# Kernel tuning notes

Measured on AMD Instinct MI355X. Metric: run time of the kernel, lower is better.

## Reference

```python
import jax, jax.numpy as jnp
import numpy as np

EMBED_DIM = 1024
NUM_HEADS = 16
D_K = EMBED_DIM // NUM_HEADS


def setup_inputs() -> dict:
    key = jax.random.key(0)
    ks = jax.random.split(key, 9)
    s = 1.0 / np.sqrt(EMBED_DIM)
    x = jax.random.normal(ks[0], (4, 2048, EMBED_DIM), dtype=jnp.float32)
    # nn.Linear weights stored as [out, in]; we keep [in, out] for x @ W
    W_q = jax.random.uniform(ks[1], (EMBED_DIM, EMBED_DIM), jnp.float32, -s, s)
    b_q = jax.random.uniform(ks[2], (EMBED_DIM,), jnp.float32, -s, s)
    W_k = jax.random.uniform(ks[3], (EMBED_DIM, EMBED_DIM), jnp.float32, -s, s)
    b_k = jax.random.uniform(ks[4], (EMBED_DIM,), jnp.float32, -s, s)
    W_v = jax.random.uniform(ks[5], (EMBED_DIM, EMBED_DIM), jnp.float32, -s, s)
    b_v = jax.random.uniform(ks[6], (EMBED_DIM,), jnp.float32, -s, s)
    W_o = jax.random.uniform(ks[7], (EMBED_DIM, EMBED_DIM), jnp.float32, -s, s)
    b_o = jax.random.uniform(ks[8], (EMBED_DIM,), jnp.float32, -s, s)
    return {"x": x, "W_q": W_q, "b_q": b_q, "W_k": W_k, "b_k": b_k,
            "W_v": W_v, "b_v": b_v, "W_o": W_o, "b_o": b_o}


def reference(x, W_q, b_q, W_k, b_k, W_v, b_v, W_o, b_o):
    B, N, _ = x.shape
    # QKV projections, split into heads: [B, H, N, d_k]
    def proj(W, b):
        return (x @ W + b).reshape(B, N, NUM_HEADS, D_K).transpose(0, 2, 1, 3)
    Q, K, V = proj(W_q, b_q), proj(W_k, b_k), proj(W_v, b_v)
    scale = 1.0 / np.sqrt(D_K).astype(np.float32)
    scores = jnp.einsum('bhqd,bhkd->bhqk', Q, K) * scale  # [B,H,N,N]
    weights = jax.nn.softmax(scores, axis=-1)
    # dropout is identity in eval mode
    attn = jnp.einsum('bhqk,bhkd->bhqd', weights, V)  # [B,H,N,d_k]
    attn = attn.transpose(0, 2, 1, 3).reshape(B, N, EMBED_DIM)
    return attn @ W_o + b_o
```

## Files before the change

### kernel.cpp

```cpp
#include <hip/hip_runtime.h>

typedef __bf16 bf16;
typedef __attribute__((ext_vector_type(8))) __bf16 bf16x8;
typedef __attribute__((ext_vector_type(4))) __bf16 bf16x4;
typedef __attribute__((ext_vector_type(4))) float f32x4;

static __device__ __forceinline__ f32x4 mfma16(bf16x8 a, bf16x8 b, f32x4 c) {
    return __builtin_amdgcn_mfma_f32_16x16x32_bf16(a, b, c, 0, 0, 0);
}

static __device__ __forceinline__ void gll16(const bf16* g, bf16* l) {
    __builtin_amdgcn_global_load_lds(
        (const __attribute__((address_space(1))) unsigned int*)g,
        (__attribute__((address_space(3))) unsigned int*)l, 16, 0, 0);
}

__global__ __launch_bounds__(256) void xcvt_kernel(
    const float* __restrict__ x, bf16* __restrict__ xb)
{
    size_t i = ((size_t)blockIdx.x * 256 + threadIdx.x) * 8;
    float4 a0 = *(const float4*)&x[i];
    float4 a1 = *(const float4*)&x[i + 4];
    bf16x8 v = {(bf16)a0.x, (bf16)a0.y, (bf16)a0.z, (bf16)a0.w,
                (bf16)a1.x, (bf16)a1.y, (bf16)a1.z, (bf16)a1.w};
    *(bf16x8*)&xb[i] = v;
}

__global__ __launch_bounds__(256) void wtrans_kernel(
    const float* __restrict__ Wq, const float* __restrict__ Wk,
    const float* __restrict__ Wv, const float* __restrict__ Wo,
    bf16* __restrict__ WTqkv, bf16* __restrict__ WTo)
{
    __shared__ bf16 tile[64][65];
    const int bid = blockIdx.x;
    const int mi = bid >> 8;
    const int t  = bid & 255;
    const int tr = t >> 4;
    const int tc = t & 15;
    const int tid = threadIdx.x;

    const float* src = (mi == 0) ? Wq : (mi == 1) ? Wk : (mi == 2) ? Wv : Wo;
    bf16* dst = (mi < 3) ? (WTqkv + (size_t)mi * 1024 * 1024) : WTo;

    #pragma unroll
    for (int i = 0; i < 16; i++) {
        int idx = i * 256 + tid;
        int rl = idx >> 6, cl = idx & 63;
        tile[rl][cl] = (bf16)src[(size_t)(tr * 64 + rl) * 1024 + tc * 64 + cl];
    }
    __syncthreads();
    #pragma unroll
    for (int i = 0; i < 16; i++) {
        int idx = i * 256 + tid;
        int rl = idx >> 6, cl = idx & 63;
        dst[(size_t)(tc * 64 + rl) * 1024 + tr * 64 + cl] = tile[cl][rl];
    }
}

__global__ void biascat_kernel(const float* __restrict__ bq, const float* __restrict__ bk,
                               const float* __restrict__ bv, float* __restrict__ dst)
{
    int i = blockIdx.x * 256 + threadIdx.x;
    if (i < 1024) dst[i] = bq[i];
    else if (i < 2048) dst[i] = bk[i - 1024];
    else dst[i] = bv[i - 2048];
}

#define QSCALE 0.18033688011112043f
__global__ __launch_bounds__(256) void gemm_bf16_kernel(
    const bf16* __restrict__ A, const bf16* __restrict__ BT,
    const float* __restrict__ bias, bf16* __restrict__ C,
    int M, int N, int K, int scaleQ)
{
    __shared__ bf16 sA[2][128 * 32];
    __shared__ bf16 sB[2][128 * 32];
    const int tid  = threadIdx.x;
    const int lane = tid & 63;
    const int wave = tid >> 6;
    const int quad = lane >> 4;
    const int l15  = lane & 15;
    const int wm = (wave >> 1) * 64;
    const int wn = (wave & 1) * 64;
    const int m0 = blockIdx.y * 128;
    const int n0 = blockIdx.x * 128;

    const f32x4 fzero = {0.f, 0.f, 0.f, 0.f};
    f32x4 acc[4][4];
    #pragma unroll
    for (int i = 0; i < 4; i++)
        #pragma unroll
        for (int j = 0; j < 4; j++) acc[i][j] = fzero;

    float bv[4];
    #pragma unroll
    for (int nc = 0; nc < 4; nc++) bv[nc] = bias[n0 + wn + nc * 16 + l15];

    const int rA = lane >> 2;
    const int cAsw = ((lane & 3) ^ ((lane >> 3) & 3)) * 8;
    const int gsw = (l15 >> 1) & 3;

#define GSTAGE(K0, BUF)                                                           \
    _Pragma("unroll")                                                             \
    for (int p = 0; p < 2; p++) {                                                 \
        int r16 = (wave * 2 + p) * 16;                                            \
        gll16(&A[(size_t)(m0 + r16 + rA) * K + (K0) + cAsw], &sA[BUF][r16 * 32]); \
        gll16(&BT[(size_t)(n0 + r16 + rA) * K + (K0) + cAsw], &sB[BUF][r16 * 32]);\
    }

#define GCOMPUTE(BUF)                                                             \
    {                                                                             \
        bf16x8 aF[4], bF[4];                                                      \
        _Pragma("unroll")                                                         \
        for (int mc = 0; mc < 4; mc++)                                            \
            aF[mc] = *(const bf16x8*)&sA[BUF][(wm + mc * 16 + l15) * 32 + ((quad ^ gsw) * 8)]; \
        _Pragma("unroll")                                                         \
        for (int nc = 0; nc < 4; nc++)                                            \
            bF[nc] = *(const bf16x8*)&sB[BUF][(wn + nc * 16 + l15) * 32 + ((quad ^ gsw) * 8)]; \
        _Pragma("unroll")                                                         \
        for (int mc = 0; mc < 4; mc++)                                            \
            _Pragma("unroll")                                                     \
            for (int nc = 0; nc < 4; nc++)                                        \
                acc[mc][nc] = mfma16(aF[mc], bF[nc], acc[mc][nc]);                \
    }

    GSTAGE(0, 0);
    __syncthreads();
    int buf = 0;
    for (int k0 = 0; k0 < K - 32; k0 += 32, buf ^= 1) {
        GSTAGE(k0 + 32, buf ^ 1);
        __builtin_amdgcn_sched_barrier(0);
        GCOMPUTE(buf);
        __syncthreads();
    }
    GCOMPUTE(buf);

    const float sc = (scaleQ && n0 < 1024) ? QSCALE : 1.0f;
    #pragma unroll
    for (int mc = 0; mc < 4; mc++) {
        #pragma unroll
        for (int reg = 0; reg < 4; reg++) {
            int row = m0 + wm + mc * 16 + quad * 4 + reg;
            size_t base = (size_t)row * N + n0 + wn;
            #pragma unroll
            for (int nc = 0; nc < 4; nc++)
                C[base + nc * 16 + l15] = (bf16)((acc[mc][nc][reg] + bv[nc]) * sc);
        }
    }
}

__global__ __launch_bounds__(256) void gemm_bf16_f32out_kernel(
    const bf16* __restrict__ A, const bf16* __restrict__ BT,
    const float* __restrict__ bias, float* __restrict__ C,
    int M, int N, int K)
{
    __shared__ bf16 sA[2][128 * 32];
    __shared__ bf16 sB[2][128 * 32];
    const int tid  = threadIdx.x;
    const int lane = tid & 63;
    const int wave = tid >> 6;
    const int quad = lane >> 4;
    const int l15  = lane & 15;
    const int wm = (wave >> 1) * 64;
    const int wn = (wave & 1) * 64;
    const int m0 = blockIdx.y * 128;
    const int n0 = blockIdx.x * 128;

    const f32x4 fzero = {0.f, 0.f, 0.f, 0.f};
    f32x4 acc[4][4];
    #pragma unroll
    for (int i = 0; i < 4; i++)
        #pragma unroll
        for (int j = 0; j < 4; j++) acc[i][j] = fzero;

    float bv[4];
    #pragma unroll
    for (int nc = 0; nc < 4; nc++) bv[nc] = bias[n0 + wn + nc * 16 + l15];

    const int rA = lane >> 2;
    const int cAsw = ((lane & 3) ^ ((lane >> 3) & 3)) * 8;
    const int gsw = (l15 >> 1) & 3;

    GSTAGE(0, 0);
    __syncthreads();
    int buf = 0;
    for (int k0 = 0; k0 < K - 32; k0 += 32, buf ^= 1) {
        GSTAGE(k0 + 32, buf ^ 1);
        __builtin_amdgcn_sched_barrier(0);
        GCOMPUTE(buf);
        __syncthreads();
    }
    GCOMPUTE(buf);

#undef GSTAGE
#undef GCOMPUTE

    #pragma unroll
    for (int mc = 0; mc < 4; mc++) {
        #pragma unroll
        for (int reg = 0; reg < 4; reg++) {
            int row = m0 + wm + mc * 16 + quad * 4 + reg;
            size_t base = (size_t)row * N + n0 + wn;
            #pragma unroll
            for (int nc = 0; nc < 4; nc++)
                C[base + nc * 16 + l15] = acc[mc][nc][reg] + bv[nc];
        }
    }
}

__global__ __launch_bounds__(256) void vtrans_kernel(
    const bf16* __restrict__ QKVp, bf16* __restrict__ Vt)
{
    __shared__ bf16 tile[64][65];
    const int bid = blockIdx.x;
    const int bh = bid >> 5;
    const int nt = bid & 31;
    const int b = bh >> 4, h = bh & 15;
    const int tid = threadIdx.x;

    #pragma unroll
    for (int i = 0; i < 16; i++) {
        int idx = i * 256 + tid;
        int rl = idx >> 6, cl = idx & 63;
        tile[rl][cl] = QKVp[(size_t)(b * 2048 + nt * 64 + rl) * 3072 + 2048 + h * 64 + cl];
    }
    __syncthreads();
    #pragma unroll
    for (int i = 0; i < 16; i++) {
        int idx = i * 256 + tid;
        int rl = idx >> 6, cl = idx & 63;
        Vt[((size_t)bh * 64 + rl) * 2048 + nt * 64 + cl] = tile[cl][rl];
    }
}

__global__ __launch_bounds__(128, 2) void attn_kernel(
    const bf16* __restrict__ QKV, const bf16* __restrict__ Vt,
    bf16* __restrict__ Opre)
{
    __shared__ bf16 sK[2][64 * 64];
    __shared__ bf16 sV[2][64 * 64];

    const int tid  = threadIdx.x;
    const int lane = tid & 63;
    const int w    = tid >> 6;
    const int quad = lane >> 4;
    const int l15  = lane & 15;
    const int bid = (blockIdx.x & 7) * 128 + (blockIdx.x >> 3);
    const int bh = bid >> 4;
    const int qt = bid & 15;
    const int b = bh >> 4, h = bh & 15;
    const int q0 = qt * 128;

    bf16x8 qF[4][2];
    #pragma unroll
    for (int g = 0; g < 4; g++) {
        size_t qrow = (size_t)(b * 2048 + q0 + w * 64 + g * 16 + l15) * 3072 + h * 64;
        qF[g][0] = *(const bf16x8*)&QKV[qrow + quad * 8];
        qF[g][1] = *(const bf16x8*)&QKV[qrow + 32 + quad * 8];
    }

    const f32x4 fzero = {0.f, 0.f, 0.f, 0.f};
    const bf16 one = (bf16)1.0f;
    const bf16x8 ones = {one, one, one, one, one, one, one, one};
    f32x4 ps[4] = {fzero, fzero, fzero, fzero};
    f32x4 o[4][4];
    #pragma unroll
    for (int g = 0; g < 4; g++)
        #pragma unroll
        for (int mt = 0; mt < 4; mt++) o[g][mt] = fzero;

    const int srow = tid >> 3, sseg = tid & 7;
    const size_t kbase = (size_t)(b * 2048) * 3072 + 1024 + h * 64;
    const size_t vbase = (size_t)bh * 64 * 2048;
    const int sgsw = sseg ^ ((srow & 3) | (((srow >> 3) & 1) << 2));

    const int swk = (l15 & 3) | (((l15 >> 2) & 1) << 2);
    const int swv = (l15 & 3) | (((l15 >> 3) & 1) << 2);

    bf16x8 stK[4], stV[4];

#define ISSUE(KEY0)                                                               \
    _Pragma("unroll")                                                             \
    for (int p = 0; p < 4; p++) {                                                 \
        int row = srow + p * 16;                                                  \
        stK[p] = *(const bf16x8*)&QKV[kbase + (size_t)((KEY0) + row) * 3072 + sseg * 8]; \
        stV[p] = *(const bf16x8*)&Vt[vbase + (size_t)row * 2048 + (KEY0) + sseg * 8];    \
    }

#define COMMIT(BUF)                                                               \
    _Pragma("unroll")                                                             \
    for (int p = 0; p < 4; p++) {                                                 \
        int row = srow + p * 16;                                                  \
        *(bf16x8*)&sK[BUF][row * 64 + sgsw * 8] = stK[p];                         \
        *(bf16x8*)&sV[BUF][row * 64 + sgsw * 8] = stV[p];                         \
    }

    auto compute_tile = [&](const bf16* sKc, const bf16* sVc) {
        bf16x8 pB[4][2];
        #pragma unroll
        for (int c = 0; c < 4; c++) {
            int kr = ((l15 >> 2) << 3) + ((c & 1) << 2) + (l15 & 3) + ((c >> 1) << 5);
            bf16x8 kA0 = *(const bf16x8*)&sKc[kr * 64 + ((quad ^ swk) * 8)];
            bf16x8 kA1 = *(const bf16x8*)&sKc[kr * 64 + (((4 + quad) ^ swk) * 8)];
            #pragma unroll
            for (int g = 0; g < 4; g++) {
                __builtin_amdgcn_s_setprio(1);
                f32x4 st = mfma16(kA0, qF[g][0], fzero);
                st = mfma16(kA1, qF[g][1], st);
                __builtin_amdgcn_s_setprio(0);
                #pragma unroll
                for (int r = 0; r < 4; r++) {
                    float p = __builtin_amdgcn_exp2f(st[r]);
                    pB[g][c >> 1][(c & 1) * 4 + r] = (bf16)p;
                }
            }
        }
        __builtin_amdgcn_s_setprio(1);
        #pragma unroll
        for (int g = 0; g < 4; g++) {
            ps[g] = mfma16(ones, pB[g][0], ps[g]);
            ps[g] = mfma16(ones, pB[g][1], ps[g]);
        }
        __builtin_amdgcn_s_setprio(0);
        #pragma unroll
        for (int mt = 0; mt < 4; mt++) {
            int vr = mt * 16 + l15;
            bf16x8 vA0 = *(const bf16x8*)&sVc[vr * 64 + ((quad ^ swv) * 8)];
            bf16x8 vA1 = *(const bf16x8*)&sVc[vr * 64 + (((4 + quad) ^ swv) * 8)];
            __builtin_amdgcn_s_setprio(1);
            #pragma unroll
            for (int g = 0; g < 4; g++) {
                o[g][mt] = mfma16(vA0, pB[g][0], o[g][mt]);
                o[g][mt] = mfma16(vA1, pB[g][1], o[g][mt]);
            }
            __builtin_amdgcn_s_setprio(0);
        }
    };

    ISSUE(0);
    COMMIT(0);
    __syncthreads();

    for (int t = 0; t < 31; t++) {
        ISSUE((t + 1) * 64);
        __builtin_amdgcn_sched_barrier(0);
        compute_tile(sK[t & 1], sV[t & 1]);
        COMMIT((t + 1) & 1);
        __syncthreads();
    }
    compute_tile(sK[1], sV[1]);

#undef ISSUE
#undef COMMIT

    #pragma unroll
    for (int g = 0; g < 4; g++) {
        float inv = 1.0f / ps[g][0];
        size_t obase = (size_t)(b * 2048 + q0 + w * 64 + g * 16 + l15) * 1024 + h * 64;
        #pragma unroll
        for (int mt = 0; mt < 4; mt++) {
            bf16x4 ov = {(bf16)(o[g][mt][0] * inv), (bf16)(o[g][mt][1] * inv),
                         (bf16)(o[g][mt][2] * inv), (bf16)(o[g][mt][3] * inv)};
            *(bf16x4*)&Opre[obase + mt * 16 + quad * 4] = ov;
        }
    }
}

extern "C" void kernel_launch(void* const* d_in, const int* in_sizes, int n_in,
                              void* d_out, int out_size, void* d_ws, size_t ws_size,
                              hipStream_t stream)
{
    const float* x  = (const float*)d_in[0];
    const float* Wq = (const float*)d_in[1];
    const float* bq = (const float*)d_in[2];
    const float* Wk = (const float*)d_in[3];
    const float* bk = (const float*)d_in[4];
    const float* Wv = (const float*)d_in[5];
    const float* bv = (const float*)d_in[6];
    const float* Wo = (const float*)d_in[7];
    const float* bo = (const float*)d_in[8];
    float* out = (float*)d_out;

    bf16* WTqkv = (bf16*)d_ws;
    bf16* WTo   = WTqkv + (size_t)3072 * 1024;
    float* bcat = (float*)(WTo + (size_t)1024 * 1024);
    bf16* QKVp  = (bf16*)(bcat + 4096);
    bf16* Vt    = QKVp + (size_t)8192 * 3072;
    bf16* Apre  = Vt + (size_t)64 * 64 * 2048;
    bf16* xb    = Apre;
    (void)ws_size; (void)n_in; (void)in_sizes; (void)out_size;

    xcvt_kernel<<<4096, 256, 0, stream>>>(x, xb);
    wtrans_kernel<<<1024, 256, 0, stream>>>(Wq, Wk, Wv, Wo, WTqkv, WTo);
    biascat_kernel<<<12, 256, 0, stream>>>(bq, bk, bv, bcat);
    gemm_bf16_kernel<<<dim3(24, 64), 256, 0, stream>>>(xb, WTqkv, bcat, QKVp, 8192, 3072, 1024, 1);
    vtrans_kernel<<<2048, 256, 0, stream>>>(QKVp, Vt);
    attn_kernel<<<1024, 128, 0, stream>>>(QKVp, Vt, Apre);
    gemm_bf16_f32out_kernel<<<dim3(8, 64), 256, 0, stream>>>(Apre, WTo, bo, out, 8192, 1024, 1024);
}
```

Measured before the change: 277.1 us.

## Merge prep kernels into one launch and interleave softmax with PV MFMAs in attention

The x conversion, weight transpose and bias concatenation kernels are combined into a single prep kernel that dispatches on block index, removing two launches. In the attention tile, the QK/exp work for the first half of keys is now followed by the rowsum and PV MFMAs for that half before the second half is computed. V fragments are loaded in batches, and the setprio toggles are hoisted to span the whole tile. This is meant to overlap exp (VALU) with MFMA work and cut priority-switch overhead, at the cost of more live registers, which may reduce occupancy.

```diff
diff --git a/kernel.cpp b/kernel.cpp
--- a/kernel.cpp
+++ b/kernel.cpp
@@ -15,55 +15,53 @@
         (__attribute__((address_space(3))) unsigned int*)l, 16, 0, 0);
 }
 
-__global__ __launch_bounds__(256) void xcvt_kernel(
-    const float* __restrict__ x, bf16* __restrict__ xb)
-{
-    size_t i = ((size_t)blockIdx.x * 256 + threadIdx.x) * 8;
-    float4 a0 = *(const float4*)&x[i];
-    float4 a1 = *(const float4*)&x[i + 4];
-    bf16x8 v = {(bf16)a0.x, (bf16)a0.y, (bf16)a0.z, (bf16)a0.w,
-                (bf16)a1.x, (bf16)a1.y, (bf16)a1.z, (bf16)a1.w};
-    *(bf16x8*)&xb[i] = v;
-}
-
-__global__ __launch_bounds__(256) void wtrans_kernel(
+__global__ __launch_bounds__(256) void prep_kernel(
+    const float* __restrict__ x, bf16* __restrict__ xb,
     const float* __restrict__ Wq, const float* __restrict__ Wk,
     const float* __restrict__ Wv, const float* __restrict__ Wo,
-    bf16* __restrict__ WTqkv, bf16* __restrict__ WTo)
+    bf16* __restrict__ WTqkv, bf16* __restrict__ WTo,
+    const float* __restrict__ bq, const float* __restrict__ bk,
+    const float* __restrict__ bv, float* __restrict__ bcat)
 {
     __shared__ bf16 tile[64][65];
     const int bid = blockIdx.x;
-    const int mi = bid >> 8;
-    const int t  = bid & 255;
-    const int tr = t >> 4;
-    const int tc = t & 15;
     const int tid = threadIdx.x;
 
-    const float* src = (mi == 0) ? Wq : (mi == 1) ? Wk : (mi == 2) ? Wv : Wo;
-    bf16* dst = (mi < 3) ? (WTqkv + (size_t)mi * 1024 * 1024) : WTo;
-
-    #pragma unroll
-    for (int i = 0; i < 16; i++) {
-        int idx = i * 256 + tid;
-        int rl = idx >> 6, cl = idx & 63;
-        tile[rl][cl] = (bf16)src[(size_t)(tr * 64 + rl) * 1024 + tc * 64 + cl];
-    }
-    __syncthreads();
-    #pragma unroll
-    for (int i = 0; i < 16; i++) {
-        int idx = i * 256 + tid;
-        int rl = idx >> 6, cl = idx & 63;
-        dst[(size_t)(tc * 64 + rl) * 1024 + tr * 64 + cl] = tile[cl][rl];
-    }
-}
-
-__global__ void biascat_kernel(const float* __restrict__ bq, const float* __restrict__ bk,
-                               const float* __restrict__ bv, float* __restrict__ dst)
-{
-    int i = blockIdx.x * 256 + threadIdx.x;
-    if (i < 1024) dst[i] = bq[i];
-    else if (i < 2048) dst[i] = bk[i - 1024];
-    else dst[i] = bv[i - 2048];
+    if (bid < 4096) {
+        size_t i = ((size_t)bid * 256 + tid) * 8;
+        float4 a0 = *(const float4*)&x[i];
+        float4 a1 = *(const float4*)&x[i + 4];
+        bf16x8 v = {(bf16)a0.x, (bf16)a0.y, (bf16)a0.z, (bf16)a0.w,
+                    (bf16)a1.x, (bf16)a1.y, (bf16)a1.z, (bf16)a1.w};
+        *(bf16x8*)&xb[i] = v;
+    } else if (bid < 5120) {
+        const int wb = bid - 4096;
+        const int mi = wb >> 8;
+        const int t  = wb & 255;
+        const int tr = t >> 4;
+        const int tc = t & 15;
+        const float* src = (mi == 0) ? Wq : (mi == 1) ? Wk : (mi == 2) ? Wv : Wo;
+        bf16* dst = (mi < 3) ? (WTqkv + (size_t)mi * 1024 * 1024) : WTo;
+
+        #pragma unroll
+        for (int i = 0; i < 16; i++) {
+            int idx = i * 256 + tid;
+            int rl = idx >> 6, cl = idx & 63;
+            tile[rl][cl] = (bf16)src[(size_t)(tr * 64 + rl) * 1024 + tc * 64 + cl];
+        }
+        __syncthreads();
+        #pragma unroll
+        for (int i = 0; i < 16; i++) {
+            int idx = i * 256 + tid;
+            int rl = idx >> 6, cl = idx & 63;
+            dst[(size_t)(tc * 64 + rl) * 1024 + tr * 64 + cl] = tile[cl][rl];
+        }
+    } else {
+        int i = (bid - 5120) * 256 + tid;
+        if (i < 1024) bcat[i] = bq[i];
+        else if (i < 2048) bcat[i] = bk[i - 1024];
+        else if (i < 3072) bcat[i] = bv[i - 2048];
+    }
 }
 
 #define QSCALE 0.18033688011112043f
@@ -296,44 +294,62 @@
 
     auto compute_tile = [&](const bf16* sKc, const bf16* sVc) {
         bf16x8 pB[4][2];
-        #pragma unroll
-        for (int c = 0; c < 4; c++) {
-            int kr = ((l15 >> 2) << 3) + ((c & 1) << 2) + (l15 & 3) + ((c >> 1) << 5);
+        __builtin_amdgcn_s_setprio(1);
+        #pragma unroll
+        for (int c = 0; c < 2; c++) {
+            int kr = ((l15 >> 2) << 3) + (c << 2) + (l15 & 3);
             bf16x8 kA0 = *(const bf16x8*)&sKc[kr * 64 + ((quad ^ swk) * 8)];
             bf16x8 kA1 = *(const bf16x8*)&sKc[kr * 64 + (((4 + quad) ^ swk) * 8)];
             #pragma unroll
             for (int g = 0; g < 4; g++) {
-                __builtin_amdgcn_s_setprio(1);
                 f32x4 st = mfma16(kA0, qF[g][0], fzero);
                 st = mfma16(kA1, qF[g][1], st);
-                __builtin_amdgcn_s_setprio(0);
                 #pragma unroll
                 for (int r = 0; r < 4; r++) {
                     float p = __builtin_amdgcn_exp2f(st[r]);
-                    pB[g][c >> 1][(c & 1) * 4 + r] = (bf16)p;
+                    pB[g][0][c * 4 + r] = (bf16)p;
                 }
             }
         }
-        __builtin_amdgcn_s_setprio(1);
-        #pragma unroll
-        for (int g = 0; g < 4; g++) {
-            ps[g] = mfma16(ones, pB[g][0], ps[g]);
-            ps[g] = mfma16(ones, pB[g][1], ps[g]);
-        }
+        bf16x8 vA0[4];
+        #pragma unroll
+        for (int mt = 0; mt < 4; mt++)
+            vA0[mt] = *(const bf16x8*)&sVc[(mt * 16 + l15) * 64 + ((quad ^ swv) * 8)];
+        #pragma unroll
+        for (int c = 0; c < 2; c++) {
+            int kr = ((l15 >> 2) << 3) + (c << 2) + (l15 & 3) + 32;
+            bf16x8 kA0 = *(const bf16x8*)&sKc[kr * 64 + ((quad ^ swk) * 8)];
+            bf16x8 kA1 = *(const bf16x8*)&sKc[kr * 64 + (((4 + quad) ^ swk) * 8)];
+            #pragma unroll
+            for (int g = 0; g < 4; g++) {
+                f32x4 st = mfma16(kA0, qF[g][0], fzero);
+                st = mfma16(kA1, qF[g][1], st);
+                #pragma unroll
+                for (int r = 0; r < 4; r++) {
+                    float p = __builtin_amdgcn_exp2f(st[r]);
+                    pB[g][1][c * 4 + r] = (bf16)p;
+                }
+            }
+        }
+        #pragma unroll
+        for (int g = 0; g < 4; g++) ps[g] = mfma16(ones, pB[g][0], ps[g]);
+        #pragma unroll
+        for (int mt = 0; mt < 4; mt++)
+            #pragma unroll
+            for (int g = 0; g < 4; g++)
+                o[g][mt] = mfma16(vA0[mt], pB[g][0], o[g][mt]);
+        bf16x8 vA1[4];
+        #pragma unroll
+        for (int mt = 0; mt < 4; mt++)
+            vA1[mt] = *(const bf16x8*)&sVc[(mt * 16 + l15) * 64 + (((4 + quad) ^ swv) * 8)];
+        #pragma unroll
+        for (int g = 0; g < 4; g++) ps[g] = mfma16(ones, pB[g][1], ps[g]);
+        #pragma unroll
+        for (int mt = 0; mt < 4; mt++)
+            #pragma unroll
+            for (int g = 0; g < 4; g++)
+                o[g][mt] = mfma16(vA1[mt], pB[g][1], o[g][mt]);
         __builtin_amdgcn_s_setprio(0);
-        #pragma unroll
-        for (int mt = 0; mt < 4; mt++) {
-            int vr = mt * 16 + l15;
-            bf16x8 vA0 = *(const bf16x8*)&sVc[vr * 64 + ((quad ^ swv) * 8)];
-            bf16x8 vA1 = *(const bf16x8*)&sVc[vr * 64 + (((4 + quad) ^ swv) * 8)];
-            __builtin_amdgcn_s_setprio(1);
-            #pragma unroll
-            for (int g = 0; g < 4; g++) {
-                o[g][mt] = mfma16(vA0, pB[g][0], o[g][mt]);
-                o[g][mt] = mfma16(vA1, pB[g][1], o[g][mt]);
-            }
-            __builtin_amdgcn_s_setprio(0);
-        }
     };
 
     ISSUE(0);
@@ -389,9 +405,8 @@
     bf16* xb    = Apre;
     (void)ws_size; (void)n_in; (void)in_sizes; (void)out_size;
 
-    xcvt_kernel<<<4096, 256, 0, stream>>>(x, xb);
-    wtrans_kernel<<<1024, 256, 0, stream>>>(Wq, Wk, Wv, Wo, WTqkv, WTo);
-    biascat_kernel<<<12, 256, 0, stream>>>(bq, bk, bv, bcat);
+    prep_kernel<<<5132, 256, 0, stream>>>(x, xb, Wq, Wk, Wv, Wo, WTqkv, WTo,
+                                          bq, bk, bv, bcat);
     gemm_bf16_kernel<<<dim3(24, 64), 256, 0, stream>>>(xb, WTqkv, bcat, QKVp, 8192, 3072, 1024, 1);
     vtrans_kernel<<<2048, 256, 0, stream>>>(QKVp, Vt);
     attn_kernel<<<1024, 128, 0, stream>>>(QKVp, Vt, Apre);
```

New measurement: 269.0 us. 1.03x faster.
